# Kernel tuning notes

Measured on AMD Instinct MI355X. Metric: run time of the kernel, lower is better.

Reference implementation:

```python
import jax, jax.numpy as jnp
import numpy as np

N_NODES = 50000
NEG_SLOPE = 0.2


def gat_conv(x, W, att_src, att_dst, b, src, dst, n):
    # x: [N, F_in], W: [F_in, H*C], att_*: [H, C], b: [H*C]
    H, C = att_src.shape
    h = (x @ W).reshape(n, H, C)                       # [N, H, C]
    a_s = (h * att_src).sum(-1)                        # [N, H]
    a_d = (h * att_dst).sum(-1)                        # [N, H]
    e = jax.nn.leaky_relu(a_s[src] + a_d[dst], NEG_SLOPE)  # [E, H]
    # segment softmax over destination node (every node has a self-loop)
    m = jax.ops.segment_max(e, dst, num_segments=n)    # [N, H]
    ex = jnp.exp(e - m[dst])
    denom = jax.ops.segment_sum(ex, dst, num_segments=n)
    alpha = ex / denom[dst]                            # [E, H]
    out = jax.ops.segment_sum(alpha[:, :, None] * h[src], dst, num_segments=n)
    return out.reshape(n, H * C) + b


def setup_inputs() -> dict:
    key = jax.random.key(0)
    ks = jax.random.split(key, 10)
    n, e = N_NODES, 1600000
    x = jax.random.normal(ks[0], (n, 128), dtype=jnp.float32)
    edge_index = jax.random.randint(ks[1], (2, e), 0, n, dtype=jnp.int64)
    s = 0.1
    return {
        "x": x,
        "edge_index": edge_index,
        "W1": jax.random.normal(ks[2], (128, 128), dtype=jnp.float32) * s,
        "att_src1": jax.random.normal(ks[3], (4, 32), dtype=jnp.float32) * s,
        "att_dst1": jax.random.normal(ks[4], (4, 32), dtype=jnp.float32) * s,
        "b1": jnp.zeros((128,), dtype=jnp.float32),
        "W2": jax.random.normal(ks[5], (128, 128), dtype=jnp.float32) * s,
        "att_src2": jax.random.normal(ks[6], (4, 32), dtype=jnp.float32) * s,
        "att_dst2": jax.random.normal(ks[7], (4, 32), dtype=jnp.float32) * s,
        "b2": jnp.zeros((128,), dtype=jnp.float32),
    }


def reference(x, edge_index, W1, att_src1, att_dst1, b1, W2, att_src2, att_dst2, b2):
    n = x.shape[0]
    loops = jnp.arange(n, dtype=edge_index.dtype)
    src = jnp.concatenate([edge_index[0], loops])  # add self-loops (PyG default)
    dst = jnp.concatenate([edge_index[1], loops])
    h = gat_conv(x, W1, att_src1, att_dst1, b1, src, dst, n)
    h = jax.nn.relu(h)
    h = gat_conv(h, W2, att_src2, att_dst2, b2, src, dst, n)
    return (h, h)
```

## Files before the change

### kernel.cpp

```cpp
#include <hip/hip_runtime.h>
#include <hip/hip_bf16.h>


#define FDIM 128
#define NHEAD 4
#define NB 512

typedef __attribute__((ext_vector_type(16))) float f32x16;
typedef __attribute__((ext_vector_type(8)))  short s16x8;

__device__ inline unsigned short f2bf(float f) {
    union { float f; unsigned u; } v; v.f = f;
    unsigned r = v.u + 0x7fff + ((v.u >> 16) & 1);
    return (unsigned short)(r >> 16);
}
__device__ inline float2 bf2f(unsigned v) {
    union { unsigned u; float f; } a, b;
    a.u = v << 16;
    b.u = v & 0xffff0000u;
    return make_float2(a.f, b.f);
}
__device__ inline void splitbf(float f, short* hi, short* lo) {
    unsigned u = __float_as_uint(f);
    float rem = f - __uint_as_float(u & 0xffff0000u);
    *hi = (short)(u >> 16);
    *lo = (short)(__float_as_uint(rem) >> 16);
}

__global__ __launch_bounds__(256) void prep_hist(const float* __restrict__ W1,
                                                 short* __restrict__ B1hi,
                                                 short* __restrict__ B1lo,
                                                 const float* __restrict__ W2,
                                                 short* __restrict__ B2hi,
                                                 short* __restrict__ B2lo,
                                                 const int* __restrict__ dst, int E,
                                                 unsigned long long magic,
                                                 int* __restrict__ bcnt) {
    __shared__ int sh[NB];
    const int t = threadIdx.x;
    const int b = blockIdx.x;
    if (b < 128) {
        const float* W = (b < 64) ? W1 : W2;
        short* Bhi = (b < 64) ? B1hi : B2hi;
        short* Blo = (b < 64) ? B1lo : B2lo;
        int e = (b & 63) * 256 + t;
        int k = e >> 7, n = e & 127;
        short hi, lo;
        splitbf(W[e], &hi, &lo);
        int idx = n * 128 + (((k >> 3) ^ (n & 15)) << 3) + (k & 7);
        Bhi[idx] = hi;
        Blo[idx] = lo;
        return;
    }
    for (int i = t; i < NB; i += 256) sh[i] = 0;
    __syncthreads();
    const int stride = (gridDim.x - 128) * 256;
    for (int i = (b - 128) * 256 + t; i < E; i += stride) {
        int bk = (int)(((unsigned long long)(unsigned)dst[i] * magic) >> 40);
        atomicAdd(&sh[bk], 1);
    }
    __syncthreads();
    for (int i = t; i < NB; i += 256)
        if (sh[i]) atomicAdd(&bcnt[i], sh[i]);
}

__global__ __launch_bounds__(256) void gemm_mfma(const float* __restrict__ A,
                                                 const short* __restrict__ Bghi,
                                                 const short* __restrict__ Bglo,
                                                 unsigned short* __restrict__ H,
                                                 const float* __restrict__ att_s,
                                                 const float* __restrict__ att_d,
                                                 float* __restrict__ a_s,
                                                 float* __restrict__ a_d, int M) {
    __shared__ short Bsm[2][16384];
    __shared__ float attsm[256];
    const int t = threadIdx.x;
    const int bm = blockIdx.x * 64;

    if (t < 128) attsm[t] = att_s[t];
    else         attsm[t] = att_d[t - 128];

    {
        const uint4* ghi = (const uint4*)Bghi;
        const uint4* glo = (const uint4*)Bglo;
        uint4* shi = (uint4*)&Bsm[0][0];
        uint4* slo = (uint4*)&Bsm[1][0];
        #pragma unroll
        for (int i = 0; i < 8; i++) {
            shi[t + i * 256] = ghi[t + i * 256];
            slo[t + i * 256] = glo[t + i * 256];
        }
    }

    const int lane = t & 63;
    const int w = t >> 6;
    const int wr = w >> 1, wc = w & 1;
    const int m  = lane & 31, h2 = lane >> 5;
    const int grow = bm + wr * 32 + m;

    s16x8 ahi[8], alo[8];
    {
        const bool ok = grow < M;
        const float* ap = A + (size_t)grow * 128 + 8 * h2;
        #pragma unroll
        for (int c = 0; c < 8; c++) {
            float ff[8];
            if (ok) {
                float4 f0 = *(const float4*)(ap + c * 16);
                float4 f1 = *(const float4*)(ap + c * 16 + 4);
                ff[0]=f0.x; ff[1]=f0.y; ff[2]=f0.z; ff[3]=f0.w;
                ff[4]=f1.x; ff[5]=f1.y; ff[6]=f1.z; ff[7]=f1.w;
            } else {
                #pragma unroll
                for (int j = 0; j < 8; j++) ff[j] = 0.f;
            }
            #pragma unroll
            for (int j = 0; j < 8; j++) {
                short hi, lo;
                splitbf(ff[j], &hi, &lo);
                ahi[c][j] = hi;
                alo[c][j] = lo;
            }
        }
    }
    __syncthreads();

    f32x16 acc[2];
    #pragma unroll
    for (int i = 0; i < 16; i++) { acc[0][i] = 0.f; acc[1][i] = 0.f; }

    #pragma unroll
    for (int ni = 0; ni < 2; ni++) {
        const int n = ni * 64 + wc * 32 + m;
        const int nbase = n * 128;
        #pragma unroll
        for (int c = 0; c < 8; c++) {
            int chunk8 = 2 * c + h2;
            int koff = ((chunk8 ^ (n & 15)) << 3);
            s16x8 bhi = *(const s16x8*)&Bsm[0][nbase + koff];
            s16x8 blo = *(const s16x8*)&Bsm[1][nbase + koff];
            acc[ni] = __builtin_amdgcn_mfma_f32_32x32x16_bf16(ahi[c], bhi, acc[ni], 0, 0, 0);
            acc[ni] = __builtin_amdgcn_mfma_f32_32x32x16_bf16(alo[c], bhi, acc[ni], 0, 0, 0);
            acc[ni] = __builtin_amdgcn_mfma_f32_32x32x16_bf16(ahi[c], blo, acc[ni], 0, 0, 0);
        }
    }

    __syncthreads();
    unsigned short* htile = (unsigned short*)&Bsm[0][0];
    #pragma unroll
    for (int ni = 0; ni < 2; ni++) {
        const int colg = ni * 64 + wc * 32 + m;
        #pragma unroll
        for (int r = 0; r < 16; r++) {
            int row = wr * 32 + (r & 3) + 8 * (r >> 2) + 4 * h2;
            htile[row * 128 + colg] = (short)f2bf(acc[ni][r]);
        }
    }
    __syncthreads();

    {
        const int r = t >> 2, q = t & 3;
        const int growr = bm + r;
        if (growr < M) {
            uint4 v0 = *(uint4*)&htile[r * 128 + q * 32];
            uint4 v1 = *(uint4*)&htile[r * 128 + q * 32 + 8];
            uint4 v2 = *(uint4*)&htile[r * 128 + q * 32 + 16];
            uint4 v3 = *(uint4*)&htile[r * 128 + q * 32 + 24];
            uint4* hg = (uint4*)(H + (size_t)growr * 128);
            hg[q * 4 + 0] = v0; hg[q * 4 + 1] = v1;
            hg[q * 4 + 2] = v2; hg[q * 4 + 3] = v3;
            unsigned uu[16] = {v0.x, v0.y, v0.z, v0.w, v1.x, v1.y, v1.z, v1.w,
                               v2.x, v2.y, v2.z, v2.w, v3.x, v3.y, v3.z, v3.w};
            float ps = 0.f, pd = 0.f;
            #pragma unroll
            for (int i = 0; i < 16; i++) {
                float2 f = bf2f(uu[i]);
                ps += f.x * attsm[q * 32 + 2 * i]       + f.y * attsm[q * 32 + 2 * i + 1];
                pd += f.x * attsm[128 + q * 32 + 2 * i] + f.y * attsm[128 + q * 32 + 2 * i + 1];
            }
            a_s[growr * NHEAD + q] = ps;
            a_d[growr * NHEAD + q] = pd;
        }
    }
}

__global__ __launch_bounds__(256) void bucket_scan(const int* __restrict__ bcnt,
                                                   int* __restrict__ bbase,
                                                   int* __restrict__ bcursor,
                                                   int* __restrict__ row_ptr,
                                                   int N, int E) {
    __shared__ int wsum[4];
    const int t = threadIdx.x, lane = t & 63, wid = t >> 6;
    int v0 = bcnt[2 * t], v1 = bcnt[2 * t + 1];
    int s = v0 + v1, incl = s;
    #pragma unroll
    for (int o = 1; o < 64; o <<= 1) {
        int u = __shfl_up(incl, o, 64);
        if (lane >= o) incl += u;
    }
    if (lane == 63) wsum[wid] = incl;
    __syncthreads();
    if (t == 0) {
        int a = 0;
        #pragma unroll
        for (int i = 0; i < 4; i++) { int x = wsum[i]; wsum[i] = a; a += x; }
    }
    __syncthreads();
    int excl = wsum[wid] + incl - s;
    bbase[2 * t] = excl;          bcursor[2 * t] = excl;
    bbase[2 * t + 1] = excl + v0; bcursor[2 * t + 1] = excl + v0;
    if (t == 0) { bbase[NB] = E; row_ptr[N] = E; }
}

__global__ __launch_bounds__(256) void partition(const int* __restrict__ src,
                                                 const int* __restrict__ dst, int E,
                                                 unsigned long long magic,
                                                 int* __restrict__ bcursor,
                                                 int2* __restrict__ ebuf) {
    __shared__ int shc[NB];
    __shared__ int shb[NB];
    __shared__ int shcur[NB];
    const int t = threadIdx.x;
    for (int i = t; i < NB; i += 256) shc[i] = 0;
    __syncthreads();
    const int e0 = blockIdx.x * 4096;
    int myb[16], mys[16], myd[16];
    #pragma unroll
    for (int u = 0; u < 16; u++) {
        int i = e0 + u * 256 + t;
        if (i < E) {
            mys[u] = src[i];
            myd[u] = dst[i];
            int b = (int)(((unsigned long long)(unsigned)myd[u] * magic) >> 40);
            myb[u] = b;
            atomicAdd(&shc[b], 1);
        } else myb[u] = -1;
    }
    __syncthreads();
    for (int i = t; i < NB; i += 256) {
        int c = shc[i];
        shcur[i] = 0;
        if (c) shb[i] = atomicAdd(&bcursor[i], c);
    }
    __syncthreads();
    #pragma unroll
    for (int u = 0; u < 16; u++) {
        if (myb[u] >= 0) {
            int o = atomicAdd(&shcur[myb[u]], 1);
            ebuf[shb[myb[u]] + o] = make_int2(mys[u], myd[u]);
        }
    }
}

__global__ __launch_bounds__(256) void build_bucket(const int2* __restrict__ ebuf,
                                                    const int* __restrict__ bbase,
                                                    int npb, int N,
                                                    int* __restrict__ row_ptr,
                                                    int* __restrict__ col,
                                                    int* __restrict__ edst) {
    __shared__ int degl[256];
    __shared__ int curl[256];
    const int b = blockIdx.x;
    const int t = threadIdx.x, lane = t & 63, wid = t >> 6;
    const int base = bbase[b];
    const int cnt = bbase[b + 1] - base;
    const int node0 = b * npb;
    for (int i = t; i < npb; i += 256) degl[i] = 0;
    __syncthreads();
    for (int i = t; i < cnt; i += 256) {
        int d = ebuf[base + i].y;
        atomicAdd(&degl[d - node0], 1);
    }
    __syncthreads();
    if (wid == 0) {
        int run = 0;
        for (int c = 0; c * 64 < npb; c++) {
            int idx = c * 64 + lane;
            int v = (idx < npb) ? degl[idx] : 0;
            int incl = v;
            #pragma unroll
            for (int o = 1; o < 64; o <<= 1) {
                int u = __shfl_up(incl, o, 64);
                if (lane >= o) incl += u;
            }
            int excl = incl - v + run;
            if (idx < npb) {
                curl[idx] = excl;
                int node = node0 + idx;
                if (node < N) row_ptr[node] = base + excl;
            }
            run += __shfl(incl, 63, 64);
        }
    }
    __syncthreads();
    for (int i = t; i < cnt; i += 256) {
        int2 ed = ebuf[base + i];
        int p = atomicAdd(&curl[ed.y - node0], 1);
        col[base + p] = ed.x;
        edst[base + p] = ed.y;
    }
}

__global__ __launch_bounds__(256) void edge_w(const int* __restrict__ col,
                                              const int* __restrict__ edst,
                                              const float4* __restrict__ as4,
                                              const float4* __restrict__ ad4,
                                              int E, float4* __restrict__ w4) {
    int i = blockIdx.x * 256 + threadIdx.x;
    if (i >= E) return;
    float4 a = as4[col[i]];
    float4 b = ad4[edst[i]];
    float ex = a.x + b.x, ey = a.y + b.y, ez = a.z + b.z, ew = a.w + b.w;
    ex = fmaxf(ex, 0.2f * ex); ey = fmaxf(ey, 0.2f * ey);
    ez = fmaxf(ez, 0.2f * ez); ew = fmaxf(ew, 0.2f * ew);
    w4[i] = make_float4(__expf(ex), __expf(ey), __expf(ez), __expf(ew));
}

__global__ __launch_bounds__(64) void aggregate(const unsigned short* __restrict__ h,
                                                const float* __restrict__ a_s,
                                                const float* __restrict__ a_d,
                                                const int* __restrict__ row_ptr,
                                                const int* __restrict__ col,
                                                const float* __restrict__ wbuf,
                                                const float* __restrict__ bias,
                                                float* __restrict__ out,
                                                float* __restrict__ out2,
                                                int n, int do_relu) {
    const int nid = blockIdx.x;
    const int c = threadIdx.x;
    const int hd = c >> 4;
    const unsigned* __restrict__ h2 = (const unsigned*)h;

    float e = a_s[nid * NHEAD + hd] + a_d[nid * NHEAD + hd];
    e = fmaxf(e, 0.2f * e);
    float den = __expf(e);
    float2 hv = bf2f(h2[(size_t)nid * 64 + c]);
    float num0 = den * hv.x, num1 = den * hv.y;

    const int beg = row_ptr[nid], end = row_ptr[nid + 1];
    int j = beg;
    for (; j + 8 <= end; j += 8) {
        int s[8];
        #pragma unroll
        for (int u = 0; u < 8; u++) s[u] = col[j + u];
        unsigned v[8]; float wv[8];
        #pragma unroll
        for (int u = 0; u < 8; u++) v[u] = h2[(size_t)s[u] * 64 + c];
        #pragma unroll
        for (int u = 0; u < 8; u++) wv[u] = wbuf[(size_t)(j + u) * 4 + hd];
        #pragma unroll
        for (int u = 0; u < 8; u++) {
            den += wv[u];
            float2 f = bf2f(v[u]);
            num0 += wv[u] * f.x;
            num1 += wv[u] * f.y;
        }
    }
    for (; j < end; j++) {
        int s = col[j];
        float wgt = wbuf[(size_t)j * 4 + hd];
        den += wgt;
        float2 f = bf2f(h2[(size_t)s * 64 + c]);
        num0 += wgt * f.x;
        num1 += wgt * f.y;
    }
    float2 bv = ((const float2*)bias)[c];
    float rd = 1.0f / den;
    float o0 = num0 * rd + bv.x;
    float o1 = num1 * rd + bv.y;
    if (do_relu) { o0 = fmaxf(o0, 0.f); o1 = fmaxf(o1, 0.f); }
    ((float2*)out)[(size_t)nid * 64 + c] = make_float2(o0, o1);
    if (out2) ((float2*)out2)[(size_t)nid * 64 + c] = make_float2(o0, o1);
}

extern "C" void kernel_launch(void* const* d_in, const int* in_sizes, int n_in,
                              void* d_out, int out_size, void* d_ws, size_t ws_size,
                              hipStream_t stream) {
    const float* x        = (const float*)d_in[0];
    const int*   edge     = (const int*)d_in[1];
    const float* W1       = (const float*)d_in[2];
    const float* att_s1   = (const float*)d_in[3];
    const float* att_d1   = (const float*)d_in[4];
    const float* b1       = (const float*)d_in[5];
    const float* W2       = (const float*)d_in[6];
    const float* att_s2   = (const float*)d_in[7];
    const float* att_d2   = (const float*)d_in[8];
    const float* b2       = (const float*)d_in[9];
    float* out = (float*)d_out;

    const int N = in_sizes[0] / FDIM;
    const int E = in_sizes[1] / 2;
    const int* src = edge;
    const int* dst = edge + E;

    const int npb = (N + NB - 1) / NB;
    const unsigned long long magic = ((1ull << 40) / (unsigned long long)npb) + 1;

    char* w = (char*)d_ws;
    size_t off = 0;
    auto alloc = [&](size_t bytes) { void* p = w + off; off = (off + bytes + 255) & ~(size_t)255; return p; };
    int*   row_ptr = (int*)alloc((size_t)(N + 1) * 4);
    int*   col     = (int*)alloc((size_t)E * 4);
    int*   edst    = (int*)alloc((size_t)E * 4);
    float* wbuf    = (float*)alloc((size_t)E * 4 * 4);
    int*   bcnt    = (int*)alloc((size_t)NB * 4);
    int*   bbase   = (int*)alloc((size_t)(NB + 1) * 4);
    int*   bcursor = (int*)alloc((size_t)NB * 4);
    unsigned short* h1 = (unsigned short*)alloc((size_t)N * FDIM * 2);
    float* hx      = (float*)alloc((size_t)N * FDIM * 4);
    float* as1     = (float*)alloc((size_t)N * NHEAD * 4);
    float* ad1     = (float*)alloc((size_t)N * NHEAD * 4);
    float* as2     = (float*)alloc((size_t)N * NHEAD * 4);
    float* ad2     = (float*)alloc((size_t)N * NHEAD * 4);
    short* Bg1hi   = (short*)alloc((size_t)128 * 128 * 2);
    short* Bg1lo   = (short*)alloc((size_t)128 * 128 * 2);
    short* Bg2hi   = (short*)alloc((size_t)128 * 128 * 2);
    short* Bg2lo   = (short*)alloc((size_t)128 * 128 * 2);
    int2*  ebuf    = (int2*)hx;
    (void)ws_size;

    hipMemsetAsync(bcnt, 0, (size_t)NB * 4, stream);
    prep_hist<<<128 + 1024, 256, 0, stream>>>(W1, Bg1hi, Bg1lo, W2, Bg2hi, Bg2lo,
                                              dst, E, magic, bcnt);
    bucket_scan<<<1, 256, 0, stream>>>(bcnt, bbase, bcursor, row_ptr, N, E);
    partition<<<(E + 4095) / 4096, 256, 0, stream>>>(src, dst, E, magic, bcursor, ebuf);
    build_bucket<<<NB, 256, 0, stream>>>(ebuf, bbase, npb, N, row_ptr, col, edst);

    const int gblocks = (N + 63) / 64;
    const int eb = (E + 255) / 256;

    gemm_mfma<<<gblocks, 256, 0, stream>>>(x, Bg1hi, Bg1lo, h1, att_s1, att_d1, as1, ad1, N);
    edge_w<<<eb, 256, 0, stream>>>(col, edst, (const float4*)as1, (const float4*)ad1,
                                   E, (float4*)wbuf);
    aggregate<<<N, 64, 0, stream>>>(h1, as1, ad1, row_ptr, col, wbuf, b1,
                                    hx, nullptr, N, 1);

    gemm_mfma<<<gblocks, 256, 0, stream>>>(hx, Bg2hi, Bg2lo, h1, att_s2, att_d2, as2, ad2, N);
    edge_w<<<eb, 256, 0, stream>>>(col, edst, (const float4*)as2, (const float4*)ad2,
                                   E, (float4*)wbuf);
    aggregate<<<N, 64, 0, stream>>>(h1, as2, ad2, row_ptr, col, wbuf, b2,
                                    out, out + (size_t)N * FDIM, N, 0);
}
```

Before: 338.1 us.

## Split features into head-pair halves and store edge weights as fp16

The projected features are stored as two half-width arrays, each holding two heads, and edge softmax weights are stored as two half2 arrays instead of float4. Each aggregate block now covers two nodes for one head pair, with adjacent blocks handling the two halves, so the gathered working set per pass is smaller and cache locality should improve. Weight traffic is halved by the fp16 storage. The costs are fp16 rounding of the exp weights, with possible overflow for large logits, and more blocks each re-reading row_ptr and col.

```diff
diff --git a/kernel.cpp b/kernel.cpp
--- a/kernel.cpp
+++ b/kernel.cpp
@@ -1,5 +1,6 @@
 #include <hip/hip_runtime.h>
 #include <hip/hip_bf16.h>
+#include <hip/hip_fp16.h>
 
 
 #define FDIM 128
@@ -67,7 +68,8 @@
 __global__ __launch_bounds__(256) void gemm_mfma(const float* __restrict__ A,
                                                  const short* __restrict__ Bghi,
                                                  const short* __restrict__ Bglo,
-                                                 unsigned short* __restrict__ H,
+                                                 unsigned short* __restrict__ H0,
+                                                 unsigned short* __restrict__ H1,
                                                  const float* __restrict__ att_s,
                                                  const float* __restrict__ att_d,
                                                  float* __restrict__ a_s,
@@ -166,9 +168,11 @@
             uint4 v1 = *(uint4*)&htile[r * 128 + q * 32 + 8];
             uint4 v2 = *(uint4*)&htile[r * 128 + q * 32 + 16];
             uint4 v3 = *(uint4*)&htile[r * 128 + q * 32 + 24];
-            uint4* hg = (uint4*)(H + (size_t)growr * 128);
-            hg[q * 4 + 0] = v0; hg[q * 4 + 1] = v1;
-            hg[q * 4 + 2] = v2; hg[q * 4 + 3] = v3;
+            unsigned short* Hp = (q < 2) ? H0 : H1;
+            uint4* hg = (uint4*)(Hp + (size_t)growr * 64);
+            const int qq = q & 1;
+            hg[qq * 4 + 0] = v0; hg[qq * 4 + 1] = v1;
+            hg[qq * 4 + 2] = v2; hg[qq * 4 + 3] = v3;
             unsigned uu[16] = {v0.x, v0.y, v0.z, v0.w, v1.x, v1.y, v1.z, v1.w,
                                v2.x, v2.y, v2.z, v2.w, v3.x, v3.y, v3.z, v3.w};
             float ps = 0.f, pd = 0.f;
@@ -305,7 +309,9 @@
                                               const int* __restrict__ edst,
                                               const float4* __restrict__ as4,
                                               const float4* __restrict__ ad4,
-                                              int E, float4* __restrict__ w4) {
+                                              int E,
+                                              __half2* __restrict__ w0,
+                                              __half2* __restrict__ w1) {
     int i = blockIdx.x * 256 + threadIdx.x;
     if (i >= E) return;
     float4 a = as4[col[i]];
@@ -313,64 +319,76 @@
     float ex = a.x + b.x, ey = a.y + b.y, ez = a.z + b.z, ew = a.w + b.w;
     ex = fmaxf(ex, 0.2f * ex); ey = fmaxf(ey, 0.2f * ey);
     ez = fmaxf(ez, 0.2f * ez); ew = fmaxf(ew, 0.2f * ew);
-    w4[i] = make_float4(__expf(ex), __expf(ey), __expf(ez), __expf(ew));
-}
-
-__global__ __launch_bounds__(64) void aggregate(const unsigned short* __restrict__ h,
+    w0[i] = __floats2half2_rn(__expf(ex), __expf(ey));
+    w1[i] = __floats2half2_rn(__expf(ez), __expf(ew));
+}
+
+__global__ __launch_bounds__(64) void aggregate(const unsigned* __restrict__ h0,
+                                                const unsigned* __restrict__ h1,
+                                                const __half2* __restrict__ w0,
+                                                const __half2* __restrict__ w1,
                                                 const float* __restrict__ a_s,
                                                 const float* __restrict__ a_d,
                                                 const int* __restrict__ row_ptr,
                                                 const int* __restrict__ col,
-                                                const float* __restrict__ wbuf,
                                                 const float* __restrict__ bias,
                                                 float* __restrict__ out,
                                                 float* __restrict__ out2,
                                                 int n, int do_relu) {
-    const int nid = blockIdx.x;
-    const int c = threadIdx.x;
-    const int hd = c >> 4;
-    const unsigned* __restrict__ h2 = (const unsigned*)h;
-
-    float e = a_s[nid * NHEAD + hd] + a_d[nid * NHEAD + hd];
+    const int b = blockIdx.x;
+    const int p = b & 1;
+    const unsigned* __restrict__ hp = p ? h1 : h0;
+    const __half2* __restrict__ wp = p ? w1 : w0;
+    const int t = threadIdx.x;
+    const int g = t >> 5;
+    const int li = t & 31;
+    const int node = (b >> 1) * 2 + g;
+    if (node >= n) return;
+    const int hd = p * 2 + (li >> 4);
+    const bool hiH = (li >> 4) != 0;
+
+    float e = a_s[node * NHEAD + hd] + a_d[node * NHEAD + hd];
     e = fmaxf(e, 0.2f * e);
     float den = __expf(e);
-    float2 hv = bf2f(h2[(size_t)nid * 64 + c]);
+    float2 hv = bf2f(hp[(size_t)node * 32 + li]);
     float num0 = den * hv.x, num1 = den * hv.y;
 
-    const int beg = row_ptr[nid], end = row_ptr[nid + 1];
+    const int beg = row_ptr[node], end = row_ptr[node + 1];
     int j = beg;
     for (; j + 8 <= end; j += 8) {
         int s[8];
         #pragma unroll
         for (int u = 0; u < 8; u++) s[u] = col[j + u];
-        unsigned v[8]; float wv[8];
-        #pragma unroll
-        for (int u = 0; u < 8; u++) v[u] = h2[(size_t)s[u] * 64 + c];
-        #pragma unroll
-        for (int u = 0; u < 8; u++) wv[u] = wbuf[(size_t)(j + u) * 4 + hd];
+        unsigned v[8]; __half2 hw[8];
+        #pragma unroll
+        for (int u = 0; u < 8; u++) v[u] = hp[(size_t)s[u] * 32 + li];
+        #pragma unroll
+        for (int u = 0; u < 8; u++) hw[u] = wp[j + u];
         #pragma unroll
         for (int u = 0; u < 8; u++) {
-            den += wv[u];
+            float wgt = hiH ? __high2float(hw[u]) : __low2float(hw[u]);
+            den += wgt;
             float2 f = bf2f(v[u]);
-            num0 += wv[u] * f.x;
-            num1 += wv[u] * f.y;
+            num0 += wgt * f.x;
+            num1 += wgt * f.y;
         }
     }
     for (; j < end; j++) {
         int s = col[j];
-        float wgt = wbuf[(size_t)j * 4 + hd];
+        __half2 hw = wp[j];
+        float wgt = hiH ? __high2float(hw) : __low2float(hw);
         den += wgt;
-        float2 f = bf2f(h2[(size_t)s * 64 + c]);
+        float2 f = bf2f(hp[(size_t)s * 32 + li]);
         num0 += wgt * f.x;
         num1 += wgt * f.y;
     }
-    float2 bv = ((const float2*)bias)[c];
+    float2 bv = ((const float2*)bias)[p * 32 + li];
     float rd = 1.0f / den;
     float o0 = num0 * rd + bv.x;
     float o1 = num1 * rd + bv.y;
     if (do_relu) { o0 = fmaxf(o0, 0.f); o1 = fmaxf(o1, 0.f); }
-    ((float2*)out)[(size_t)nid * 64 + c] = make_float2(o0, o1);
-    if (out2) ((float2*)out2)[(size_t)nid * 64 + c] = make_float2(o0, o1);
+    ((float2*)out)[(size_t)node * 64 + p * 32 + li] = make_float2(o0, o1);
+    if (out2) ((float2*)out2)[(size_t)node * 64 + p * 32 + li] = make_float2(o0, o1);
 }
 
 extern "C" void kernel_launch(void* const* d_in, const int* in_sizes, int n_in,
@@ -402,11 +420,13 @@
     int*   row_ptr = (int*)alloc((size_t)(N + 1) * 4);
     int*   col     = (int*)alloc((size_t)E * 4);
     int*   edst    = (int*)alloc((size_t)E * 4);
-    float* wbuf    = (float*)alloc((size_t)E * 4 * 4);
+    __half2* w0    = (__half2*)alloc((size_t)E * 4);
+    __half2* w1    = (__half2*)alloc((size_t)E * 4);
     int*   bcnt    = (int*)alloc((size_t)NB * 4);
     int*   bbase   = (int*)alloc((size_t)(NB + 1) * 4);
     int*   bcursor = (int*)alloc((size_t)NB * 4);
-    unsigned short* h1 = (unsigned short*)alloc((size_t)N * FDIM * 2);
+    unsigned short* h0 = (unsigned short*)alloc((size_t)N * 64 * 2);
+    unsigned short* h1 = (unsigned short*)alloc((size_t)N * 64 * 2);
     float* hx      = (float*)alloc((size_t)N * FDIM * 4);
     float* as1     = (float*)alloc((size_t)N * NHEAD * 4);
     float* ad1     = (float*)alloc((size_t)N * NHEAD * 4);
@@ -428,16 +448,21 @@
 
     const int gblocks = (N + 63) / 64;
     const int eb = (E + 255) / 256;
-
-    gemm_mfma<<<gblocks, 256, 0, stream>>>(x, Bg1hi, Bg1lo, h1, att_s1, att_d1, as1, ad1, N);
+    const int ablocks = ((N + 1) / 2) * 2;
+
+    gemm_mfma<<<gblocks, 256, 0, stream>>>(x, Bg1hi, Bg1lo, h0, h1,
+                                           att_s1, att_d1, as1, ad1, N);
     edge_w<<<eb, 256, 0, stream>>>(col, edst, (const float4*)as1, (const float4*)ad1,
-                                   E, (float4*)wbuf);
-    aggregate<<<N, 64, 0, stream>>>(h1, as1, ad1, row_ptr, col, wbuf, b1,
-                                    hx, nullptr, N, 1);
-
-    gemm_mfma<<<gblocks, 256, 0, stream>>>(hx, Bg2hi, Bg2lo, h1, att_s2, att_d2, as2, ad2, N);
+                                   E, w0, w1);
+    aggregate<<<ablocks, 64, 0, stream>>>((const unsigned*)h0, (const unsigned*)h1,
+                                          w0, w1, as1, ad1, row_ptr, col, b1,
+                                          hx, nullptr, N, 1);
+
+    gemm_mfma<<<gblocks, 256, 0, stream>>>(hx, Bg2hi, Bg2lo, h0, h1,
+                                           att_s2, att_d2, as2, ad2, N);
     edge_w<<<eb, 256, 0, stream>>>(col, edst, (const float4*)as2, (const float4*)ad2,
-                                   E, (float4*)wbuf);
-    aggregate<<<N, 64, 0, stream>>>(h1, as2, ad2, row_ptr, col, wbuf, b2,
-                                    out, out + (size_t)N * FDIM, N, 0);
-}
+                                   E, w0, w1);
+    aggregate<<<ablocks, 64, 0, stream>>>((const unsigned*)h0, (const unsigned*)h1,
+                                          w0, w1, as2, ad2, row_ptr, col, b2,
+                                          out, out + (size_t)N * FDIM, N, 0);
+}
```

Result: no change. 338.0 us (-0.0%).
